# Kernel optimization log

Measured on AMD Instinct MI355X. Metric: run time of the kernel, lower is better.

## Reference

```python
import jax, jax.numpy as jnp
import numpy as np

B, C, P, T = 256, 248, 50, 4
H = 8
D = C // H          # 31, used for the attention scale (self.d ** -0.5)
DH = D * T          # 124 == dim_head of RelPosEmb1DAISummer
FFD = 16
EPS = 1e-5


def _bn(x, g, b):
    # BatchNorm2d with batch statistics over (N, H, W) per channel
    m = x.mean(axis=(0, 2, 3), keepdims=True)
    v = x.var(axis=(0, 2, 3), keepdims=True)
    return (x - m) * jax.lax.rsqrt(v + EPS) * g[None, :, None, None] + b[None, :, None, None]


def _conv(x, w, b, pw):
    # kernel is (1, kw): 'same' padding only along the last (t) axis
    y = jax.lax.conv_general_dilated(x, w, (1, 1), ((0, 0), (pw, pw)),
                                     dimension_numbers=('NCHW', 'OIHW', 'NCHW'))
    return y + b[None, :, None, None]


def _rel_to_abs(x):
    # x: [b, h, l, 2l-1] -> [b, h, l, l] (Bottleneck-Transformer trick)
    b, h, l, _ = x.shape
    x = jnp.pad(x, ((0, 0), (0, 0), (0, 0), (0, 1)))           # b h l 2l
    x = x.reshape(b, h, 2 * l * l)
    x = jnp.pad(x, ((0, 0), (0, 0), (0, l - 1)))
    x = x.reshape(b, h, l + 1, 2 * l - 1)
    return x[:, :, :l, l - 1:]


def _forward(x, w_qkv, b_qkv, rel_emb, g1, beta1, w_c1, bc1, w_c2, bc2,
             g_cfe, beta_cfe, w_c3, bc3, g2, beta2):
    b, c, p, t = x.shape
    h, d = H, c // H
    dh = d * t
    # 1x1 conv qkv projection
    qkv = jnp.einsum('bcpt,oc->bopt', x, w_qkv) + b_qkv[None, :, None, None]
    qkv = qkv.reshape(b, 3, h, d, p, t)
    q = qkv[:, 0].transpose(0, 1, 3, 2, 4).reshape(b, h, p, dh)   # b h p (d t)
    k = qkv[:, 1].transpose(0, 1, 2, 4, 3).reshape(b, h, dh, p)   # b h (d t) p
    v = qkv[:, 2].transpose(0, 1, 3, 2, 4).reshape(b, h, p, dh)
    dots = jnp.matmul(q, k)                                       # b h p p
    bias = _rel_to_abs(jnp.einsum('bhpd,rd->bhpr', q, rel_emb))   # shared-head rel bias
    attn = jax.nn.softmax((dots + bias) * (d ** -0.5), axis=-1)   # scale AFTER bias, d=31
    out = jnp.matmul(attn, v)                                     # b h p dh
    out = out.reshape(b, h, p, d, t).transpose(0, 1, 3, 2, 4).reshape(b, c, p, t)
    # residual + BN1
    x = _bn(out + x, g1, beta1)
    # CFE: two parallel convs, concat, BN, ELU, 1x1 conv (dropout = identity, eval)
    y = jnp.concatenate([_conv(x, w_c1, bc1, 1), _conv(x, w_c2, bc2, 2)], axis=1)
    y = jax.nn.elu(_bn(y, g_cfe, beta_cfe))
    y = _conv(y, w_c3, bc3, 0)
    # residual + BN2
    return _bn(y + x, g2, beta2)


def setup_inputs() -> dict:
    key = jax.random.key(0)
    ks = jax.random.split(key, 8)
    rn = lambda k, sh, s=1.0: jax.random.normal(k, sh, dtype=jnp.float32) * s
    return dict(
        x=rn(ks[0], (B, C, P, T)),
        w_qkv=rn(ks[1], (3 * C, C), 0.05), b_qkv=jnp.zeros((3 * C,), jnp.float32),
        rel_emb=rn(ks[2], (2 * P - 1, DH), DH ** -0.5),
        g1=jnp.ones((C,), jnp.float32), beta1=jnp.zeros((C,), jnp.float32),
        w_c1=rn(ks[3], (FFD // 2, C, 1, 3), 0.05), bc1=jnp.zeros((FFD // 2,), jnp.float32),
        w_c2=rn(ks[4], (FFD // 2, C, 1, 5), 0.05), bc2=jnp.zeros((FFD // 2,), jnp.float32),
        g_cfe=jnp.ones((FFD,), jnp.float32), beta_cfe=jnp.zeros((FFD,), jnp.float32),
        w_c3=rn(ks[5], (C, FFD, 1, 1), 0.05), bc3=jnp.zeros((C,), jnp.float32),
        g2=jnp.ones((C,), jnp.float32), beta2=jnp.zeros((C,), jnp.float32),
    )


def reference(x, w_qkv, b_qkv, rel_emb, g1, beta1, w_c1, bc1, w_c2, bc2,
              g_cfe, beta_cfe, w_c3, bc3, g2, beta2):
    return _forward(x, w_qkv, b_qkv, rel_emb, g1, beta1, w_c1, bc1, w_c2, bc2,
                    g_cfe, beta_cfe, w_c3, bc3, g2, beta2)
```

## Files before the change

### kernel.cpp

```cpp
#include <hip/hip_runtime.h>

#define B_ 256
#define C_ 248
#define P_ 50
#define T_ 4
#define H_ 8
#define D_ 31
#define DH_ 124
#define PT_ 200
#define O3_ 744

typedef __attribute__((ext_vector_type(8))) short short8v;
typedef __attribute__((ext_vector_type(4))) float f32x4;

__device__ __forceinline__ float bf2f(unsigned short u) {
  union { unsigned int i; float f; } v; v.i = ((unsigned int)u) << 16; return v.f;
}
__device__ __forceinline__ unsigned short f2bf(float f) {
  union { float f; unsigned int i; } v; v.f = f;
  unsigned int r = v.i + 0x7fffu + ((v.i >> 16) & 1u);
  return (unsigned short)(r >> 16);
}

__global__ void relcvt_kernel(const float* __restrict__ rel, unsigned short* __restrict__ out) {
  int i = blockIdx.x * 256 + threadIdx.x;
  if (i < 112 * 128) {
    int r = i >> 7, k = i & 127;
    out[i] = (r < 99 && k < DH_) ? f2bf(rel[r * DH_ + k]) : (unsigned short)0;
  }
}

__global__ void wcvt_kernel(const float* __restrict__ w, unsigned short* __restrict__ wbf) {
  int i = blockIdx.x * 256 + threadIdx.x;
  if (i < 768 * 64) {
    int o = i >> 6, c = (i & 63) * 4;
    ushort4 val = make_ushort4(0, 0, 0, 0);
    if (o < O3_ && c < C_) {
      float4 wv = *(const float4*)(w + (size_t)o * C_ + c);
      val.x = f2bf(wv.x); val.y = f2bf(wv.y); val.z = f2bf(wv.z); val.w = f2bf(wv.w);
    }
    *(ushort4*)(wbf + (size_t)o * 256 + c) = val;
  }
}

__global__ __launch_bounds__(256) void xt_kernel(const float* __restrict__ x,
                                                 unsigned short* __restrict__ xT) {
  __shared__ float xs[64 * 65];
  const int tid = threadIdx.x;
  const int pt0 = (blockIdx.x & 3) * 64;
  const int c0 = (blockIdx.x >> 2) * 64;
  const int b = blockIdx.y;
#pragma unroll
  for (int pass = 0; pass < 4; ++pass) {
    int row = pass * 16 + (tid >> 4);
    int ptl4 = (tid & 15) * 4;
    int c = c0 + row, pt = pt0 + ptl4;
    float4 v = make_float4(0.f, 0.f, 0.f, 0.f);
    if (c < C_) {
      const float* src = x + ((size_t)b * C_ + c) * PT_ + pt;
      if (pt + 3 < PT_) v = *(const float4*)src;
      else {
        if (pt + 0 < PT_) v.x = src[0];
        if (pt + 1 < PT_) v.y = src[1];
        if (pt + 2 < PT_) v.z = src[2];
        if (pt + 3 < PT_) v.w = src[3];
      }
    }
    xs[row * 65 + ptl4 + 0] = v.x; xs[row * 65 + ptl4 + 1] = v.y;
    xs[row * 65 + ptl4 + 2] = v.z; xs[row * 65 + ptl4 + 3] = v.w;
  }
  __syncthreads();
#pragma unroll
  for (int pass = 0; pass < 4; ++pass) {
    int ptl = pass * 16 + (tid >> 4);
    int cl4 = (tid & 15) * 4;
    int pt = pt0 + ptl;
    if (pt < 208) {
      ushort4 pk;
      pk.x = f2bf(xs[(cl4 + 0) * 65 + ptl]);
      pk.y = f2bf(xs[(cl4 + 1) * 65 + ptl]);
      pk.z = f2bf(xs[(cl4 + 2) * 65 + ptl]);
      pk.w = f2bf(xs[(cl4 + 3) * 65 + ptl]);
      *(ushort4*)(xT + ((size_t)b * 208 + pt) * 256 + c0 + cl4) = pk;
    }
  }
}

__global__ __launch_bounds__(256) void qkv_mfma_kernel(
    const unsigned short* __restrict__ xT, const unsigned short* __restrict__ wbf,
    const float* __restrict__ bias,
    unsigned short* __restrict__ q_ws, unsigned short* __restrict__ k_ws,
    unsigned short* __restrict__ v_ws) {
  const int tid = threadIdx.x;
  const int w = tid >> 6, l = tid & 63;
  const int lr = l & 15, lk = (l >> 4) * 8;
  const int b = blockIdx.y;
  const int o_w = blockIdx.x * 128 + w * 32;
  const unsigned short* xb = xT + (size_t)b * 208 * 256;

  const f32x4 zf = {0.f, 0.f, 0.f, 0.f};
  f32x4 acc0[13], acc1[13];
#pragma unroll
  for (int m = 0; m < 13; ++m) { acc0[m] = zf; acc1[m] = zf; }

#pragma unroll
  for (int ks = 0; ks < 8; ++ks) {
    int k0 = ks * 32 + lk;
    short8v b0 = *(const short8v*)(wbf + (size_t)(o_w + lr) * 256 + k0);
    short8v b1 = *(const short8v*)(wbf + (size_t)(o_w + 16 + lr) * 256 + k0);
#pragma unroll
    for (int m = 0; m < 13; ++m) {
      short8v a = *(const short8v*)(xb + (size_t)(m * 16 + lr) * 256 + k0);
      acc0[m] = __builtin_amdgcn_mfma_f32_16x16x32_bf16(a, b0, acc0[m], 0, 0, 0);
      acc1[m] = __builtin_amdgcn_mfma_f32_16x16x32_bf16(a, b1, acc1[m], 0, 0, 0);
    }
  }
#pragma unroll
  for (int n = 0; n < 2; ++n) {
    int o = o_w + n * 16 + lr;
    if (o < O3_) {
      float bo = bias[o];
      int wi = o / C_;
      int rem = o - wi * C_;
      int h = rem / D_;
      int d = rem - h * D_;
      unsigned short* dst = (wi == 0) ? q_ws : (wi == 1) ? k_ws : v_ws;
      size_t rowb = ((size_t)b * H_ + h) * P_;
#pragma unroll
      for (int m = 0; m < 13; ++m) {
        int p = 4 * m + (l >> 4);
        if (p < P_) {
          f32x4 av = (n == 0) ? acc0[m] : acc1[m];
          ushort4 pk;
          pk.x = f2bf(av[0] + bo); pk.y = f2bf(av[1] + bo);
          pk.z = f2bf(av[2] + bo); pk.w = f2bf(av[3] + bo);
          *(ushort4*)(dst + (rowb + p) * DH_ + d * T_) = pk;
        }
      }
    }
  }
}

__global__ __launch_bounds__(256) void attn_kernel(
    const unsigned short* __restrict__ q_ws, const unsigned short* __restrict__ k_ws,
    const unsigned short* __restrict__ v_ws, const unsigned short* __restrict__ relp,
    const float* __restrict__ x, float* __restrict__ pre1) {
  __shared__ __align__(16) unsigned short Qs[64 * 128];
  __shared__ __align__(16) unsigned short Ks[64 * 128];
  __shared__ __align__(16) unsigned short Vt[128 * 64];
  __shared__ __align__(16) unsigned short Ps[64 * 64];
  __shared__ __align__(16) unsigned short brs[64 * 112];
  const int tid = threadIdx.x;
  const int bh = blockIdx.x, b = bh >> 3, h = bh & 7;
  const size_t off = (size_t)bh * (P_ * DH_);

  {
    float4 z = make_float4(0.f, 0.f, 0.f, 0.f);
    float4* z1 = (float4*)Qs; float4* z2 = (float4*)Ks; float4* z3 = (float4*)Vt;
    for (int i = tid; i < 1024; i += 256) { z1[i] = z; z2[i] = z; z3[i] = z; }
  }
  __syncthreads();
  const float scale = 0.17960530202677491f;
  for (int i = tid; i < 1550; i += 256) {
    int p = i / 31, kq = (i - p * 31) * 4;
    ushort4 qv = *(const ushort4*)(q_ws + off + p * DH_ + kq);
    qv.x = f2bf(bf2f(qv.x) * scale); qv.y = f2bf(bf2f(qv.y) * scale);
    qv.z = f2bf(bf2f(qv.z) * scale); qv.w = f2bf(bf2f(qv.w) * scale);
    *(ushort4*)((char*)Qs + ((p * 256 + kq * 2) ^ ((p & 7) << 4))) = qv;
    ushort4 kv = *(const ushort4*)(k_ws + off + p * DH_ + kq);
    *(ushort4*)((char*)Ks + ((p * 256 + kq * 2) ^ ((p & 7) << 4))) = kv;
    ushort4 vv = *(const ushort4*)(v_ws + off + p * DH_ + kq);
    unsigned short ve[4] = {vv.x, vv.y, vv.z, vv.w};
#pragma unroll
    for (int e = 0; e < 4; ++e) {
      int dh = kq + e;
      *(unsigned short*)((char*)Vt + ((dh * 128 + p * 2) ^ ((dh & 7) << 4))) = ve[e];
    }
  }
  __syncthreads();

  const int w = tid >> 6, l = tid & 63;
  const int lr = l & 15;
  const int lk = (l >> 4) * 8;
  const int arow = 16 * w + lr;
  const int prow0 = 16 * w + (l >> 4) * 4;

  const f32x4 zf = {0.f, 0.f, 0.f, 0.f};
  f32x4 accS[4]; f32x4 accR[7];
#pragma unroll
  for (int n = 0; n < 4; ++n) accS[n] = zf;
#pragma unroll
  for (int n = 0; n < 7; ++n) accR[n] = zf;

#pragma unroll
  for (int ks = 0; ks < 4; ++ks) {
    int k0 = ks * 32 + lk;
    short8v a = *(const short8v*)((const char*)Qs + ((arow * 256 + 2 * k0) ^ ((arow & 7) << 4)));
#pragma unroll
    for (int n = 0; n < 4; ++n) {
      int brow = 16 * n + lr;
      short8v bb = *(const short8v*)((const char*)Ks + ((brow * 256 + 2 * k0) ^ ((brow & 7) << 4)));
      accS[n] = __builtin_amdgcn_mfma_f32_16x16x32_bf16(a, bb, accS[n], 0, 0, 0);
    }
#pragma unroll
    for (int n = 0; n < 7; ++n) {
      int rrow = 16 * n + lr;
      short8v bb = *(const short8v*)(relp + rrow * 128 + k0);
      accR[n] = __builtin_amdgcn_mfma_f32_16x16x32_bf16(a, bb, accR[n], 0, 0, 0);
    }
  }
#pragma unroll
  for (int n = 0; n < 7; ++n)
#pragma unroll
    for (int r = 0; r < 4; ++r)
      brs[(prow0 + r) * 112 + 16 * n + lr] = f2bf(accR[n][r]);
  __syncthreads();

  float sv[4][4];
#pragma unroll
  for (int n = 0; n < 4; ++n)
#pragma unroll
    for (int r = 0; r < 4; ++r) {
      int p = prow0 + r, j = 16 * n + lr;
      if (p < P_ && j < P_)
        sv[n][r] = accS[n][r] + bf2f(brs[p * 112 + (49 + j - p)]);
      else
        sv[n][r] = -1e30f;
    }
#pragma unroll
  for (int r = 0; r < 4; ++r) {
    float mm = fmaxf(fmaxf(sv[0][r], sv[1][r]), fmaxf(sv[2][r], sv[3][r]));
    mm = fmaxf(mm, __shfl_xor(mm, 1));
    mm = fmaxf(mm, __shfl_xor(mm, 2));
    mm = fmaxf(mm, __shfl_xor(mm, 4));
    mm = fmaxf(mm, __shfl_xor(mm, 8));
    float ss = 0.f;
#pragma unroll
    for (int n = 0; n < 4; ++n) { float e = __expf(sv[n][r] - mm); sv[n][r] = e; ss += e; }
    ss += __shfl_xor(ss, 1); ss += __shfl_xor(ss, 2);
    ss += __shfl_xor(ss, 4); ss += __shfl_xor(ss, 8);
    float inv = 1.f / ss;
#pragma unroll
    for (int n = 0; n < 4; ++n) sv[n][r] *= inv;
  }
#pragma unroll
  for (int n = 0; n < 4; ++n)
#pragma unroll
    for (int r = 0; r < 4; ++r) {
      int p = prow0 + r, j = 16 * n + lr;
      *(unsigned short*)((char*)Ps + ((p * 128 + 2 * j) ^ ((p & 7) << 4))) = f2bf(sv[n][r]);
    }
  __syncthreads();

  f32x4 accO[8];
#pragma unroll
  for (int n = 0; n < 8; ++n) accO[n] = zf;
#pragma unroll
  for (int ks = 0; ks < 2; ++ks) {
    int j0 = ks * 32 + lk;
    short8v a = *(const short8v*)((const char*)Ps + ((arow * 128 + 2 * j0) ^ ((arow & 7) << 4)));
#pragma unroll
    for (int n = 0; n < 8; ++n) {
      int vrow = 16 * n + lr;
      short8v bb = *(const short8v*)((const char*)Vt + ((vrow * 128 + 2 * j0) ^ ((vrow & 7) << 4)));
      accO[n] = __builtin_amdgcn_mfma_f32_16x16x32_bf16(a, bb, accO[n], 0, 0, 0);
    }
  }
#pragma unroll
  for (int n = 0; n < 8; ++n) {
    int dh = 16 * n + lr;
    if (dh < DH_) {
      int c = h * D_ + (dh >> 2), t = dh & 3;
#pragma unroll
      for (int r = 0; r < 4; ++r) {
        int p = prow0 + r;
        if (p < P_) {
          size_t idx = (((size_t)b * C_ + c) * P_ + p) * T_ + t;
          pre1[idx] = accO[n][r] + x[idx];
        }
      }
    }
  }
}

__global__ __launch_bounds__(256) void bnstat_kernel(
    const float* __restrict__ t, const float* __restrict__ g, const float* __restrict__ be,
    float* __restrict__ a, float* __restrict__ bs, int nch) {
  const int c = blockIdx.x;
  const int tid = threadIdx.x;
  const float* base = t + ((size_t)tid * nch + c) * PT_;
  float s = 0.f, s2 = 0.f;
  for (int i = 0; i < PT_; i += 4) {
    float4 v = *(const float4*)(base + i);
    s += v.x + v.y + v.z + v.w;
    s2 += v.x*v.x + v.y*v.y + v.z*v.z + v.w*v.w;
  }
#pragma unroll
  for (int off = 32; off > 0; off >>= 1) {
    s += __shfl_down(s, off);
    s2 += __shfl_down(s2, off);
  }
  __shared__ float r1[4], r2[4];
  if ((tid & 63) == 0) { r1[tid>>6] = s; r2[tid>>6] = s2; }
  __syncthreads();
  if (tid == 0) {
    s = r1[0]+r1[1]+r1[2]+r1[3];
    s2 = r2[0]+r2[1]+r2[2]+r2[3];
    const float inv = 1.f / (float)(B_ * PT_);
    float m = s * inv;
    float var = s2 * inv - m * m;
    float ai = g[c] * rsqrtf(var + 1e-5f);
    a[c] = ai;
    bs[c] = be[c] - m * ai;
  }
}

__global__ __launch_bounds__(256) void p1t_kernel(const float* __restrict__ pre1,
                                                  unsigned short* __restrict__ p1T) {
  __shared__ float xs[64][205];
  const int b = blockIdx.x;
  const int tid = threadIdx.x;
  for (int c0 = 0; c0 < C_; c0 += 64) {
    int R = (C_ - c0 < 64) ? (C_ - c0) : 64;
    __syncthreads();
    for (int e = tid; e < R * 50; e += 256) {
      int row = e / 50, pq = e - (e / 50) * 50;
      float4 v = *(const float4*)(pre1 + ((size_t)b * C_ + c0 + row) * PT_ + pq * 4);
      xs[row][pq*4+0]=v.x; xs[row][pq*4+1]=v.y; xs[row][pq*4+2]=v.z; xs[row][pq*4+3]=v.w;
    }
    __syncthreads();
    for (int u = tid; u < 50 * R; u += 256) {
      int p = u / R, cl = u - (u / R) * R;
      ushort4 pk;
      pk.x = f2bf(xs[cl][p*4+0]); pk.y = f2bf(xs[cl][p*4+1]);
      pk.z = f2bf(xs[cl][p*4+2]); pk.w = f2bf(xs[cl][p*4+3]);
      *(ushort4*)(p1T + ((size_t)b*50 + p) * 1024 + (c0+cl)*4) = pk;
    }
  }
  for (int u = tid; u < 50 * 8; u += 256) {
    int p = u >> 3, g = u & 7;
    ushort4 val = make_ushort4(0,0,0,0);
    if (g == 0) val.x = 0x3F80;
    *(ushort4*)(p1T + ((size_t)b*50 + p) * 1024 + 992 + g*4) = val;
  }
}

__global__ __launch_bounds__(256) void wcfe_kernel(
    const float* __restrict__ w1, const float* __restrict__ bc1,
    const float* __restrict__ w2, const float* __restrict__ bc2,
    const float* __restrict__ a1, const float* __restrict__ b1,
    unsigned short* __restrict__ Wbig) {
  const int n = blockIdx.x;
  const int f = n >> 2, t = n & 3;
  const int tid = threadIdx.x;
  __shared__ float red[256];
  float partial = 0.f;
  if (tid < C_) {
    int c = tid;
    float tv[4];
    float tsum = 0.f;
#pragma unroll
    for (int tp = 0; tp < 4; ++tp) {
      int dt = tp - t;
      float v = 0.f;
      if (f < 8) { if (dt >= -1 && dt <= 1) v = w1[(f * C_ + c) * 3 + dt + 1]; }
      else       { if (dt >= -2 && dt <= 2) v = w2[((f - 8) * C_ + c) * 5 + dt + 2]; }
      tv[tp] = v; tsum += v;
    }
    float ac = a1[c];
#pragma unroll
    for (int tp = 0; tp < 4; ++tp)
      Wbig[n * 1024 + c * 4 + tp] = f2bf(ac * tv[tp]);
    partial = b1[c] * tsum;
  } else {
#pragma unroll
    for (int tp = 0; tp < 4; ++tp) {
      int col = tid * 4 + tp;
      if (col > 992 && col < 1024) Wbig[n * 1024 + col] = 0;
    }
  }
  red[tid] = partial;
  __syncthreads();
  for (int s = 128; s > 0; s >>= 1) {
    if (tid < s) red[tid] += red[tid + s];
    __syncthreads();
  }
  if (tid == 0) {
    float bias = (f < 8) ? bc1[f] : bc2[f - 8];
    Wbig[n * 1024 + 992] = f2bf(bias + red[0]);
  }
}

__global__ __launch_bounds__(256) void cfe12g_kernel(
    const unsigned short* __restrict__ p1T, const unsigned short* __restrict__ Wbig,
    float* __restrict__ y16) {
  const int tid = threadIdx.x;
  const int w = tid >> 6, l = tid & 63;
  const int lr = l & 15, lk = (l >> 4) * 8;
  const int m0 = blockIdx.x * 32;
  const f32x4 zf = {0.f, 0.f, 0.f, 0.f};
  f32x4 acc0 = zf, acc1 = zf;
  const unsigned short* wrow = Wbig + (size_t)(w * 16 + lr) * 1024;
#pragma unroll
  for (int ks = 0; ks < 32; ++ks) {
    int k0 = ks * 32 + lk;
    short8v bfr = *(const short8v*)(wrow + k0);
    short8v a0 = *(const short8v*)(p1T + (size_t)(m0 + lr) * 1024 + k0);
    short8v a1v = *(const short8v*)(p1T + (size_t)(m0 + 16 + lr) * 1024 + k0);
    acc0 = __builtin_amdgcn_mfma_f32_16x16x32_bf16(a0, bfr, acc0, 0, 0, 0);
    acc1 = __builtin_amdgcn_mfma_f32_16x16x32_bf16(a1v, bfr, acc1, 0, 0, 0);
  }
  const int n = w * 16 + lr, f = n >> 2, tt = n & 3;
#pragma unroll
  for (int mt = 0; mt < 2; ++mt) {
    f32x4 av = (mt == 0) ? acc0 : acc1;
#pragma unroll
    for (int r = 0; r < 4; ++r) {
      int m = m0 + mt * 16 + (l >> 4) * 4 + r;
      int b = m / 50, p = m - (m / 50) * 50;
      y16[((size_t)b * 16 + f) * PT_ + p * 4 + tt] = av[r];
    }
  }
}

__global__ __launch_bounds__(256) void cfe3_kernel(
    const float* __restrict__ y16, const float* __restrict__ ac, const float* __restrict__ bcf,
    const float* __restrict__ w3, const float* __restrict__ bc3,
    const float* __restrict__ pre1, const float* __restrict__ a1, const float* __restrict__ b1,
    float* __restrict__ pre2) {
  const int b = blockIdx.x;
  const int tid = threadIdx.x;
  __shared__ float zs[16][PT_];
  __shared__ float w3s[C_][16];
  for (int i = tid; i < C_*16; i += 256) w3s[i >> 4][i & 15] = w3[i];
  for (int e = tid; e < 16*PT_; e += 256) {
    int f = e / PT_, pt = e - f * PT_;
    float v = y16[((size_t)b*16 + f) * PT_ + pt] * ac[f] + bcf[f];
    zs[f][pt] = (v > 0.f) ? v : (__expf(v) - 1.f);
  }
  __syncthreads();
  for (int e = tid; e < C_ * P_; e += 256) {
    int c = e / P_, p = e - (e / P_) * P_;
    float b3 = bc3[c];
    float4 o = make_float4(b3, b3, b3, b3);
#pragma unroll
    for (int f = 0; f < 16; ++f) {
      float wv = w3s[c][f];
      float4 z = *(const float4*)&zs[f][p*4];
      o.x += wv * z.x; o.y += wv * z.y; o.z += wv * z.z; o.w += wv * z.w;
    }
    size_t idx = (((size_t)b * C_ + c) * P_ + p) * T_;
    float4 xr = *(const float4*)(pre1 + idx);
    float a1c = a1[c], b1c = b1[c];
    o.x += xr.x * a1c + b1c;
    o.y += xr.y * a1c + b1c;
    o.z += xr.z * a1c + b1c;
    o.w += xr.w * a1c + b1c;
    *(float4*)(pre2 + idx) = o;
  }
}

__global__ __launch_bounds__(256) void bnapply_kernel(
    const float* __restrict__ pre2, const float* __restrict__ a, const float* __restrict__ bs,
    float* __restrict__ out) {
  int i = blockIdx.x * 256 + threadIdx.x;
  if (i < (B_*C_*PT_)/4) {
    int row = (i * 4) / PT_;
    int c = row % C_;
    float4 v = *(const float4*)(pre2 + (size_t)i * 4);
    float ai = a[c], bi = bs[c];
    float4 o = make_float4(v.x*ai+bi, v.y*ai+bi, v.z*ai+bi, v.w*ai+bi);
    *(float4*)(out + (size_t)i * 4) = o;
  }
}

extern "C" void kernel_launch(void* const* d_in, const int* in_sizes, int n_in,
                              void* d_out, int out_size, void* d_ws, size_t ws_size,
                              hipStream_t stream) {
  const float* x        = (const float*)d_in[0];
  const float* w_qkv    = (const float*)d_in[1];
  const float* b_qkv    = (const float*)d_in[2];
  const float* rel      = (const float*)d_in[3];
  const float* g1       = (const float*)d_in[4];
  const float* beta1    = (const float*)d_in[5];
  const float* w_c1     = (const float*)d_in[6];
  const float* bc1      = (const float*)d_in[7];
  const float* w_c2     = (const float*)d_in[8];
  const float* bc2      = (const float*)d_in[9];
  const float* g_cfe    = (const float*)d_in[10];
  const float* beta_cfe = (const float*)d_in[11];
  const float* w_c3     = (const float*)d_in[12];
  const float* bc3      = (const float*)d_in[13];
  const float* g2       = (const float*)d_in[14];
  const float* beta2    = (const float*)d_in[15];
  float* out = (float*)d_out;
  char* ws = (char*)d_ws;

  unsigned short* q_ws  = (unsigned short*)(ws);
  unsigned short* k_ws  = (unsigned short*)(ws + 25395200);
  unsigned short* v_ws  = (unsigned short*)(ws + 50790400);
  float* pre1           = (float*)(ws + 76185600);
  unsigned short* xT    = (unsigned short*)(ws + 76185600);
  unsigned short* wbf   = (unsigned short*)(ws + 76185600 + 27262976);
  float* y16            = (float*)(ws + 126976000);
  unsigned short* relp  = (unsigned short*)(ws + 130252800);
  unsigned short* Wbig  = (unsigned short*)(ws + 130281472);
  float* st             = (float*)(ws + 130412544);
  float* a1 = st, *b1 = st + 256, *acf = st + 512, *bcf = st + 544, *a2 = st + 576, *b2 = st + 832;
  unsigned short* p1T   = (unsigned short*)ws;
  float* pre2           = (float*)ws;

  relcvt_kernel<<<56, 256, 0, stream>>>(rel, relp);
  wcvt_kernel<<<192, 256, 0, stream>>>(w_qkv, wbf);
  xt_kernel<<<dim3(16, 256), 256, 0, stream>>>(x, xT);
  qkv_mfma_kernel<<<dim3(6, 256), 256, 0, stream>>>(xT, wbf, b_qkv, q_ws, k_ws, v_ws);
  attn_kernel<<<2048, 256, 0, stream>>>(q_ws, k_ws, v_ws, relp, x, pre1);
  bnstat_kernel<<<248, 256, 0, stream>>>(pre1, g1, beta1, a1, b1, C_);
  p1t_kernel<<<256, 256, 0, stream>>>(pre1, p1T);
  wcfe_kernel<<<64, 256, 0, stream>>>(w_c1, bc1, w_c2, bc2, a1, b1, Wbig);
  cfe12g_kernel<<<400, 256, 0, stream>>>(p1T, Wbig, y16);
  bnstat_kernel<<<16, 256, 0, stream>>>(y16, g_cfe, beta_cfe, acf, bcf, 16);
  cfe3_kernel<<<256, 256, 0, stream>>>(y16, acf, bcf, w_c3, bc3, pre1, a1, b1, pre2);
  bnstat_kernel<<<248, 256, 0, stream>>>(pre2, g2, beta2, a2, b2, C_);
  bnapply_kernel<<<12400, 256, 0, stream>>>(pre2, a2, b2, out);
}
```

Baseline: 433.7 us.

## Fuse QKV projection into attention kernel, writing Q/K/V directly to LDS

Removes the separate QKV GEMM kernel and its bf16 Q/K/V workspace round trip. Each attention block now computes its own head's Q, K and V slice from the transposed input via MFMA and scatters the results, with bias and scaling applied, into the swizzled shared-memory tiles. Block indices are also remapped so that the blocks of one batch sample land on the same XCD, improving L2 reuse of xT. The cost is that every head block reloads the full xT row for its sample, and the accumulators raise register pressure.

```diff
diff --git a/kernel.cpp b/kernel.cpp
--- a/kernel.cpp
+++ b/kernel.cpp
@@ -86,64 +86,9 @@
   }
 }
 
-__global__ __launch_bounds__(256) void qkv_mfma_kernel(
+__global__ __launch_bounds__(256) void fused_qa_kernel(
     const unsigned short* __restrict__ xT, const unsigned short* __restrict__ wbf,
-    const float* __restrict__ bias,
-    unsigned short* __restrict__ q_ws, unsigned short* __restrict__ k_ws,
-    unsigned short* __restrict__ v_ws) {
-  const int tid = threadIdx.x;
-  const int w = tid >> 6, l = tid & 63;
-  const int lr = l & 15, lk = (l >> 4) * 8;
-  const int b = blockIdx.y;
-  const int o_w = blockIdx.x * 128 + w * 32;
-  const unsigned short* xb = xT + (size_t)b * 208 * 256;
-
-  const f32x4 zf = {0.f, 0.f, 0.f, 0.f};
-  f32x4 acc0[13], acc1[13];
-#pragma unroll
-  for (int m = 0; m < 13; ++m) { acc0[m] = zf; acc1[m] = zf; }
-
-#pragma unroll
-  for (int ks = 0; ks < 8; ++ks) {
-    int k0 = ks * 32 + lk;
-    short8v b0 = *(const short8v*)(wbf + (size_t)(o_w + lr) * 256 + k0);
-    short8v b1 = *(const short8v*)(wbf + (size_t)(o_w + 16 + lr) * 256 + k0);
-#pragma unroll
-    for (int m = 0; m < 13; ++m) {
-      short8v a = *(const short8v*)(xb + (size_t)(m * 16 + lr) * 256 + k0);
-      acc0[m] = __builtin_amdgcn_mfma_f32_16x16x32_bf16(a, b0, acc0[m], 0, 0, 0);
-      acc1[m] = __builtin_amdgcn_mfma_f32_16x16x32_bf16(a, b1, acc1[m], 0, 0, 0);
-    }
-  }
-#pragma unroll
-  for (int n = 0; n < 2; ++n) {
-    int o = o_w + n * 16 + lr;
-    if (o < O3_) {
-      float bo = bias[o];
-      int wi = o / C_;
-      int rem = o - wi * C_;
-      int h = rem / D_;
-      int d = rem - h * D_;
-      unsigned short* dst = (wi == 0) ? q_ws : (wi == 1) ? k_ws : v_ws;
-      size_t rowb = ((size_t)b * H_ + h) * P_;
-#pragma unroll
-      for (int m = 0; m < 13; ++m) {
-        int p = 4 * m + (l >> 4);
-        if (p < P_) {
-          f32x4 av = (n == 0) ? acc0[m] : acc1[m];
-          ushort4 pk;
-          pk.x = f2bf(av[0] + bo); pk.y = f2bf(av[1] + bo);
-          pk.z = f2bf(av[2] + bo); pk.w = f2bf(av[3] + bo);
-          *(ushort4*)(dst + (rowb + p) * DH_ + d * T_) = pk;
-        }
-      }
-    }
-  }
-}
-
-__global__ __launch_bounds__(256) void attn_kernel(
-    const unsigned short* __restrict__ q_ws, const unsigned short* __restrict__ k_ws,
-    const unsigned short* __restrict__ v_ws, const unsigned short* __restrict__ relp,
+    const float* __restrict__ bias, const unsigned short* __restrict__ relp,
     const float* __restrict__ x, float* __restrict__ pre1) {
   __shared__ __align__(16) unsigned short Qs[64 * 128];
   __shared__ __align__(16) unsigned short Ks[64 * 128];
@@ -151,41 +96,81 @@
   __shared__ __align__(16) unsigned short Ps[64 * 64];
   __shared__ __align__(16) unsigned short brs[64 * 112];
   const int tid = threadIdx.x;
-  const int bh = blockIdx.x, b = bh >> 3, h = bh & 7;
-  const size_t off = (size_t)bh * (P_ * DH_);
+  const int xcd = blockIdx.x & 7, slot = blockIdx.x >> 3;
+  const int b = xcd * 32 + (slot >> 3), h = slot & 7;
+  const unsigned short* xb = xT + (size_t)b * 208 * 256;
+  const int w = tid >> 6, l = tid & 63;
+  const int lr = l & 15, lk = (l >> 4) * 8;
+  const int mstart = (w == 0) ? 0 : (1 + 3 * w);
+  const int mcount = (w == 0) ? 4 : 3;
+  const float scale = 0.17960530202677491f;
 
   {
     float4 z = make_float4(0.f, 0.f, 0.f, 0.f);
     float4* z1 = (float4*)Qs; float4* z2 = (float4*)Ks; float4* z3 = (float4*)Vt;
     for (int i = tid; i < 1024; i += 256) { z1[i] = z; z2[i] = z; z3[i] = z; }
   }
-  __syncthreads();
-  const float scale = 0.17960530202677491f;
-  for (int i = tid; i < 1550; i += 256) {
-    int p = i / 31, kq = (i - p * 31) * 4;
-    ushort4 qv = *(const ushort4*)(q_ws + off + p * DH_ + kq);
-    qv.x = f2bf(bf2f(qv.x) * scale); qv.y = f2bf(bf2f(qv.y) * scale);
-    qv.z = f2bf(bf2f(qv.z) * scale); qv.w = f2bf(bf2f(qv.w) * scale);
-    *(ushort4*)((char*)Qs + ((p * 256 + kq * 2) ^ ((p & 7) << 4))) = qv;
-    ushort4 kv = *(const ushort4*)(k_ws + off + p * DH_ + kq);
-    *(ushort4*)((char*)Ks + ((p * 256 + kq * 2) ^ ((p & 7) << 4))) = kv;
-    ushort4 vv = *(const ushort4*)(v_ws + off + p * DH_ + kq);
-    unsigned short ve[4] = {vv.x, vv.y, vv.z, vv.w};
-#pragma unroll
-    for (int e = 0; e < 4; ++e) {
-      int dh = kq + e;
-      *(unsigned short*)((char*)Vt + ((dh * 128 + p * 2) ^ ((dh & 7) << 4))) = ve[e];
-    }
-  }
-  __syncthreads();
-
-  const int w = tid >> 6, l = tid & 63;
-  const int lr = l & 15;
-  const int lk = (l >> 4) * 8;
+
+  const f32x4 zf = {0.f, 0.f, 0.f, 0.f};
+  f32x4 acc[4][6];
+#pragma unroll
+  for (int mi = 0; mi < 4; ++mi)
+#pragma unroll
+    for (int nt = 0; nt < 6; ++nt) acc[mi][nt] = zf;
+
+#pragma unroll
+  for (int ks = 0; ks < 8; ++ks) {
+    int k0 = ks * 32 + lk;
+    short8v bfr[6];
+#pragma unroll
+    for (int nt = 0; nt < 6; ++nt) {
+      int orow = (nt >> 1) * 248 + h * 31 + (nt & 1) * 16 + lr;
+      bfr[nt] = *(const short8v*)(wbf + (size_t)orow * 256 + k0);
+    }
+#pragma unroll
+    for (int mi = 0; mi < 4; ++mi) {
+      if (mi < mcount) {
+        short8v a = *(const short8v*)(xb + (size_t)((mstart + mi) * 16 + lr) * 256 + k0);
+#pragma unroll
+        for (int nt = 0; nt < 6; ++nt)
+          acc[mi][nt] = __builtin_amdgcn_mfma_f32_16x16x32_bf16(a, bfr[nt], acc[mi][nt], 0, 0, 0);
+      }
+    }
+  }
+  __syncthreads();
+#pragma unroll
+  for (int mi = 0; mi < 4; ++mi) {
+    if (mi < mcount) {
+#pragma unroll
+      for (int nt = 0; nt < 6; ++nt) {
+        int d = (nt & 1) * 16 + lr;
+        if (d < D_) {
+          int wi = nt >> 1;
+          float bo = bias[wi * C_ + h * D_ + d];
+#pragma unroll
+          for (int r = 0; r < 4; ++r) {
+            int pt = (mstart + mi) * 16 + (l >> 4) * 4 + r;
+            int p = pt >> 2, t = pt & 3;
+            if (p < P_) {
+              float val = acc[mi][nt][r] + bo;
+              int dh = d * 4 + t;
+              if (wi == 0)
+                *(unsigned short*)((char*)Qs + ((p * 256 + dh * 2) ^ ((p & 7) << 4))) = f2bf(val * scale);
+              else if (wi == 1)
+                *(unsigned short*)((char*)Ks + ((p * 256 + dh * 2) ^ ((p & 7) << 4))) = f2bf(val);
+              else
+                *(unsigned short*)((char*)Vt + ((dh * 128 + p * 2) ^ ((dh & 7) << 4))) = f2bf(val);
+            }
+          }
+        }
+      }
+    }
+  }
+  __syncthreads();
+
   const int arow = 16 * w + lr;
   const int prow0 = 16 * w + (l >> 4) * 4;
 
-  const f32x4 zf = {0.f, 0.f, 0.f, 0.f};
   f32x4 accS[4]; f32x4 accR[7];
 #pragma unroll
   for (int n = 0; n < 4; ++n) accS[n] = zf;
@@ -496,25 +481,21 @@
   float* out = (float*)d_out;
   char* ws = (char*)d_ws;
 
-  unsigned short* q_ws  = (unsigned short*)(ws);
-  unsigned short* k_ws  = (unsigned short*)(ws + 25395200);
-  unsigned short* v_ws  = (unsigned short*)(ws + 50790400);
+  unsigned short* xT    = (unsigned short*)(ws);
+  unsigned short* wbf   = (unsigned short*)(ws + 27262976);
+  unsigned short* p1T   = (unsigned short*)(ws + 27656192);
   float* pre1           = (float*)(ws + 76185600);
-  unsigned short* xT    = (unsigned short*)(ws + 76185600);
-  unsigned short* wbf   = (unsigned short*)(ws + 76185600 + 27262976);
   float* y16            = (float*)(ws + 126976000);
   unsigned short* relp  = (unsigned short*)(ws + 130252800);
   unsigned short* Wbig  = (unsigned short*)(ws + 130281472);
   float* st             = (float*)(ws + 130412544);
   float* a1 = st, *b1 = st + 256, *acf = st + 512, *bcf = st + 544, *a2 = st + 576, *b2 = st + 832;
-  unsigned short* p1T   = (unsigned short*)ws;
   float* pre2           = (float*)ws;
 
   relcvt_kernel<<<56, 256, 0, stream>>>(rel, relp);
   wcvt_kernel<<<192, 256, 0, stream>>>(w_qkv, wbf);
   xt_kernel<<<dim3(16, 256), 256, 0, stream>>>(x, xT);
-  qkv_mfma_kernel<<<dim3(6, 256), 256, 0, stream>>>(xT, wbf, b_qkv, q_ws, k_ws, v_ws);
-  attn_kernel<<<2048, 256, 0, stream>>>(q_ws, k_ws, v_ws, relp, x, pre1);
+  fused_qa_kernel<<<2048, 256, 0, stream>>>(xT, wbf, b_qkv, relp, x, pre1);
   bnstat_kernel<<<248, 256, 0, stream>>>(pre1, g1, beta1, a1, b1, C_);
   p1t_kernel<<<256, 256, 0, stream>>>(pre1, p1T);
   wcfe_kernel<<<64, 256, 0, stream>>>(w_c1, bc1, w_c2, bc2, a1, b1, Wbig);
```

New measurement: 398.8 us. 8.1% less time.
